# Kernel tuning notes

Hardware: AMD Instinct MI355X
Metric: run time of the kernel (lower is better)

Reference implementation:

```python
import jax, jax.numpy as jnp
import numpy as np

D = 192      # d_model
DE = 96      # d_edge
H = 8        # n_heads
DH = D // H  # d_head = 24
DF = 2 * D   # ff hidden = 384
N = 25000
E = 400000


def _layernorm(x, s, b, eps=1e-5):
    m = jnp.mean(x, axis=-1, keepdims=True)
    v = jnp.var(x, axis=-1, keepdims=True)
    return (x - m) * jax.lax.rsqrt(v + eps) * s + b


def setup_inputs() -> dict:
    key = jax.random.key(0)
    ks = jax.random.split(key, 12)
    sc = lambda d: 1.0 / np.sqrt(d)
    inp = {
        "x": jax.random.normal(ks[0], (N, D), jnp.float32),
        "edge_feat": jax.random.normal(ks[1], (E, DE), jnp.float32),
        "edge_index": jax.random.randint(ks[2], (2, E), 0, N, jnp.int64),
        # attention projections (stored [d_in, d_out], applied as x @ W)
        "Wq": jax.random.normal(ks[3], (D, D), jnp.float32) * sc(D),
        "Wk": jax.random.normal(ks[4], (D, D), jnp.float32) * sc(D),
        "Wv": jax.random.normal(ks[5], (D, D), jnp.float32) * sc(D),
        "We": jax.random.normal(ks[6], (DE, H), jnp.float32) * sc(DE),
        "Wo": jax.random.normal(ks[7], (D, D), jnp.float32) * sc(D),
        "bo": jnp.zeros((D,), jnp.float32),
        "Wg": jax.random.normal(ks[8], (2 * D, D), jnp.float32) * sc(2 * D),
        "bg": jnp.zeros((D,), jnp.float32),
        "ln1_s": jnp.ones((D,), jnp.float32),
        "ln1_b": jnp.zeros((D,), jnp.float32),
        "Wf1": jax.random.normal(ks[9], (D, DF), jnp.float32) * sc(D),
        "bf1": jnp.zeros((DF,), jnp.float32),
        "Wf2": jax.random.normal(ks[10], (DF, D), jnp.float32) * sc(DF),
        "bf2": jnp.zeros((D,), jnp.float32),
        "ln2_s": jnp.ones((D,), jnp.float32),
        "ln2_b": jnp.zeros((D,), jnp.float32),
    }
    return inp


def reference(x, edge_feat, edge_index, Wq, Wk, Wv, We, Wo, bo, Wg, bg,
              ln1_s, ln1_b, Wf1, bf1, Wf2, bf2, ln2_s, ln2_b):
    src, dst = edge_index[0], edge_index[1]
    n = x.shape[0]
    # per-edge gathered projections: [E, H, DH]
    q = (x[dst] @ Wq).reshape(-1, H, DH)
    k = (x[src] @ Wk).reshape(-1, H, DH)
    v = (x[src] @ Wv).reshape(-1, H, DH)
    score = jnp.sum(q * k, axis=-1) / np.sqrt(DH) + edge_feat @ We  # [E, H]
    # segment softmax over incoming edges of each dst node
    mx = jax.ops.segment_max(score, dst, num_segments=n)           # [N, H]
    alpha = jnp.exp(score - mx[dst])                                # [E, H]
    den = jax.ops.segment_sum(alpha, dst, num_segments=n)          # [N, H]
    num = jax.ops.segment_sum(alpha[..., None] * v, dst, num_segments=n)  # [N, H, DH]
    agg = (num / (den[:, :, None] + 1e-8)).reshape(n, D)
    o = agg @ Wo + bo
    g = jax.nn.sigmoid(jnp.concatenate([o, x], axis=-1) @ Wg + bg)
    y = _layernorm(g * o + (1.0 - g) * x, ln1_s, ln1_b)
    ff = jax.nn.silu(y @ Wf1 + bf1) @ Wf2 + bf2
    return _layernorm(y + ff, ln2_s, ln2_b)
```

## Files before the change

kernel.cpp:

```cpp
#include <hip/hip_runtime.h>
#include <cstdint>
#include <cstddef>

#define LOG2E 1.4426950408889634f

constexpr int Dm  = 192;
constexpr int DEe = 96;

typedef unsigned short u16;
typedef __attribute__((ext_vector_type(8))) short short8v;
typedef __attribute__((ext_vector_type(4))) float f32x4;

__device__ __forceinline__ u16 f2bf(float f) {
    uint32_t u = __builtin_bit_cast(uint32_t, f);
    uint32_t r = (u + 0x7FFF + ((u >> 16) & 1)) >> 16;
    return (u16)r;
}
__device__ __forceinline__ float bf2f(u16 h) {
    uint32_t u = ((uint32_t)h) << 16;
    return __builtin_bit_cast(float, u);
}
__device__ __forceinline__ uint32_t cvtpk_bf16(float lo, float hi) {
    uint32_t r;
    asm("v_cvt_pk_bf16_f32 %0, %1, %2" : "=v"(r) : "v"(lo), "v"(hi));
    return r;
}

__global__ void zero_ints(int* __restrict__ p, int n) {
    int i = blockIdx.x * blockDim.x + threadIdx.x;
    if (i < n) p[i] = 0;
}

__global__ __launch_bounds__(1024) void scan_kernel(const int* __restrict__ deg, int N,
                                                    int* __restrict__ offs) {
    __shared__ int sp[1024];
    int t = threadIdx.x;
    int per = (N + 1023) >> 10;
    int base = t * per;
    int sum = 0;
    for (int i = 0; i < per; ++i) {
        int idx = base + i;
        if (idx < N) sum += deg[idx];
    }
    sp[t] = sum;
    __syncthreads();
    for (int off = 1; off < 1024; off <<= 1) {
        int v = (t >= off) ? sp[t - off] : 0;
        __syncthreads();
        sp[t] += v;
        __syncthreads();
    }
    int run = sp[t] - sum;
    for (int i = 0; i < per; ++i) {
        int idx = base + i;
        if (idx < N) { offs[idx] = run; run += deg[idx]; }
    }
    if (t == 1023) offs[N] = sp[1023];
}

__global__ __launch_bounds__(256) void prepA(
    const int* __restrict__ ei, int E,
    const float* __restrict__ x, int n4, u16* __restrict__ xb,
    const float* __restrict__ Wq, const float* __restrict__ Wk,
    const float* __restrict__ Wv, const float* __restrict__ Wo,
    const float* __restrict__ Wg, const float* __restrict__ Wf1,
    const float* __restrict__ Wf2,
    u16* __restrict__ Wqkvt, u16* __restrict__ Wot,
    u16* __restrict__ Wgt, u16* __restrict__ Wf1t, u16* __restrict__ Wf2t,
    int* __restrict__ deg)
{
    int i = blockIdx.x * 256 + threadIdx.x;
    if (i < E) {
        atomicAdd(&deg[ei[E + i]], 1);
        return;
    }
    i -= E;
    if (i < n4) {
        float4 v = ((const float4*)x)[i];
        uint32_t p0 = cvtpk_bf16(v.x, v.y);
        uint32_t p1 = cvtpk_bf16(v.z, v.w);
        ushort4 o;
        o.x = (u16)(p0 & 0xffff); o.y = (u16)(p0 >> 16);
        o.z = (u16)(p1 & 0xffff); o.w = (u16)(p1 >> 16);
        ((ushort4*)xb)[i] = o;
        return;
    }
    int idx = i - n4;
    if (idx < 110592) {
        int n = idx / 192, k = idx % 192;
        const float* W = n < 192 ? Wq : (n < 384 ? Wk : Wv);
        Wqkvt[idx] = f2bf(W[(size_t)k * 192 + (n % 192)]);
    } else if (idx < 147456) {
        int j = idx - 110592;
        int n = j / 192, k = j % 192;
        Wot[j] = f2bf(Wo[(size_t)k * 192 + n]);
    } else if (idx < 221184) {
        int j = idx - 147456;
        int n = j / 384, k = j % 384;
        Wgt[j] = f2bf(Wg[(size_t)k * 192 + n]);
    } else if (idx < 294912) {
        int j = idx - 221184;
        int n = j / 192, k = j % 192;
        Wf1t[j] = f2bf(Wf1[(size_t)k * 384 + n]);
    } else if (idx < 368640) {
        int j = idx - 294912;
        int n = j / 384, k = j % 384;
        Wf2t[j] = f2bf(Wf2[(size_t)k * 192 + n]);
    }
}

__global__ __launch_bounds__(256) void phaseC(
    int EB,
    const int* __restrict__ ei, int E,
    const float* __restrict__ ef, const float* __restrict__ We,
    const int* __restrict__ offs, int* __restrict__ cur,
    float* __restrict__ scb, int* __restrict__ sbuf,
    const u16* __restrict__ xb, int M, int gm64,
    const u16* __restrict__ Wt, u16* __restrict__ qkvb)
{
    int bid = blockIdx.x;
    int tid = threadIdx.x;
    if (bid < EB) {
        __shared__ float We_s[DEe * 8];
        __shared__ float ef_s[32][100];
        for (int i = tid; i < DEe * 8; i += 256) We_s[i] = We[i];
        int e0 = bid * 32;
        #pragma unroll
        for (int rep = 0; rep < 3; ++rep) {
            int idx = tid + 256 * rep;
            int el = idx / 24, c4 = idx % 24;
            int e = e0 + el;
            float4 v = make_float4(0.f, 0.f, 0.f, 0.f);
            if (e < E) v = *(const float4*)&ef[(size_t)e * DEe + c4 * 4];
            *(float4*)&ef_s[el][c4 * 4] = v;
        }
        __syncthreads();
        int el = tid >> 3, h = tid & 7;
        int e = e0 + el;
        if (e >= E) return;
        float epj = 0.f;
        #pragma unroll 8
        for (int i = 0; i < DEe; ++i) epj += ef_s[el][i] * We_s[i * 8 + h];

        int lane = tid & 63;
        int pos = 0;
        if (h == 0) {
            int dst = ei[E + e];
            pos = offs[dst] + atomicAdd(&cur[dst], 1);
        }
        pos = __shfl(pos, lane & 56, 64);
        scb[(size_t)pos * 8 + h] = epj * LOG2E;
        if (h == 0) sbuf[pos] = ei[e];
        return;
    }

    int qb = bid - EB;
    int m0 = (qb % gm64) * 64, n0 = (qb / gm64) * 192;
    int w = tid >> 6, lane = tid & 63;
    int c16 = lane & 15, hi2 = lane >> 4, kof = hi2 * 8;

    int rcm[4];
    #pragma unroll
    for (int mr = 0; mr < 4; ++mr) {
        int r = m0 + mr * 16 + c16;
        rcm[mr] = r < M ? r : M - 1;
    }

    f32x4 acc[4][3];
    #pragma unroll
    for (int mr = 0; mr < 4; ++mr)
        #pragma unroll
        for (int nr = 0; nr < 3; ++nr) acc[mr][nr] = (f32x4)(0.f);

    #pragma unroll 1
    for (int ks = 0; ks < 6; ++ks) {
        short8v af[4], bfr[3];
        #pragma unroll
        for (int mr = 0; mr < 4; ++mr)
            af[mr] = *(const short8v*)(xb + (size_t)rcm[mr] * 192 + ks * 32 + kof);
        #pragma unroll
        for (int nr = 0; nr < 3; ++nr)
            bfr[nr] = *(const short8v*)(Wt + (size_t)(n0 + w * 48 + nr * 16 + c16) * 192 + ks * 32 + kof);
        #pragma unroll
        for (int mr = 0; mr < 4; ++mr)
            #pragma unroll
            for (int nr = 0; nr < 3; ++nr)
                acc[mr][nr] = __builtin_amdgcn_mfma_f32_16x16x32_bf16(
                    af[mr], bfr[nr], acc[mr][nr], 0, 0, 0);
    }

    #pragma unroll
    for (int mr = 0; mr < 4; ++mr)
        #pragma unroll
        for (int nr = 0; nr < 3; ++nr) {
            uint32_t p0 = cvtpk_bf16(acc[mr][nr][0], acc[mr][nr][1]);
            uint32_t p1 = cvtpk_bf16(acc[mr][nr][2], acc[mr][nr][3]);
            int r0 = m0 + mr * 16 + hi2 * 4;
            int col = n0 + w * 48 + nr * 16 + c16;
            if (r0     < M) qkvb[(size_t)(r0    ) * 576 + col] = (u16)(p0 & 0xffff);
            if (r0 + 1 < M) qkvb[(size_t)(r0 + 1) * 576 + col] = (u16)(p0 >> 16);
            if (r0 + 2 < M) qkvb[(size_t)(r0 + 2) * 576 + col] = (u16)(p1 & 0xffff);
            if (r0 + 3 < M) qkvb[(size_t)(r0 + 3) * 576 + col] = (u16)(p1 >> 16);
        }
}

__global__ __launch_bounds__(256) void agg_fused(
    const u16* __restrict__ qkv, const float* __restrict__ scb,
    const int* __restrict__ sbuf, const int* __restrict__ offs,
    int N, u16* __restrict__ aggb)
{
    int node = blockIdx.x * 4 + (threadIdx.x >> 6);
    if (node >= N) return;
    int lane = threadIdx.x & 63;
    int h = lane >> 3;
    int di = (3 * lane) >> 1;
    int odd = lane & 1;

    int beg = offs[node], end = offs[node + 1];
    u16* og = aggb + (size_t)node * Dm;
    int b0 = 3 * lane;
    if (beg >= end) {
        og[b0] = 0; og[b0 + 1] = 0; og[b0 + 2] = 0;
        return;
    }

    const uint32_t* qrow = (const uint32_t*)(qkv + (size_t)node * 576);
    uint32_t qd0 = qrow[di], qd1 = qrow[di + 1];
    float q0, q1, q2;
    if (!odd) { q0 = bf2f(qd0 & 0xffff); q1 = bf2f(qd0 >> 16); q2 = bf2f(qd1 & 0xffff); }
    else      { q0 = bf2f(qd0 >> 16);    q1 = bf2f(qd1 & 0xffff); q2 = bf2f(qd1 >> 16); }

    auto clampi = [&](int i) { return i < end ? i : end - 1; };

    float den = 0.f, a0 = 0.f, a1 = 0.f, a2 = 0.f;

    uint32_t ck[2][2], cv[2][2]; float cep[2];
    uint32_t nk[2][2], nv[2][2]; float nep[2];
    int s0, s1;

    {
        int p00 = clampi(beg),     p01 = clampi(beg + 1);
        int p10 = clampi(beg + 2), p11 = clampi(beg + 3);
        int sA = sbuf[p00], sB = sbuf[p01], sC = sbuf[p10], sD = sbuf[p11];
        const uint32_t* r;
        r = (const uint32_t*)(qkv + (size_t)sA * 576 + 192);
        ck[0][0] = r[di]; ck[0][1] = r[di + 1];
        r = (const uint32_t*)(qkv + (size_t)sA * 576 + 384);
        cv[0][0] = r[di]; cv[0][1] = r[di + 1];
        r = (const uint32_t*)(qkv + (size_t)sB * 576 + 192);
        ck[1][0] = r[di]; ck[1][1] = r[di + 1];
        r = (const uint32_t*)(qkv + (size_t)sB * 576 + 384);
        cv[1][0] = r[di]; cv[1][1] = r[di + 1];
        r = (const uint32_t*)(qkv + (size_t)sC * 576 + 192);
        nk[0][0] = r[di]; nk[0][1] = r[di + 1];
        r = (const uint32_t*)(qkv + (size_t)sC * 576 + 384);
        nv[0][0] = r[di]; nv[0][1] = r[di + 1];
        r = (const uint32_t*)(qkv + (size_t)sD * 576 + 192);
        nk[1][0] = r[di]; nk[1][1] = r[di + 1];
        r = (const uint32_t*)(qkv + (size_t)sD * 576 + 384);
        nv[1][0] = r[di]; nv[1][1] = r[di + 1];
        cep[0] = scb[(size_t)p00 * 8 + h]; cep[1] = scb[(size_t)p01 * 8 + h];
        nep[0] = scb[(size_t)p10 * 8 + h]; nep[1] = scb[(size_t)p11 * 8 + h];
        s0 = sbuf[clampi(beg + 4)]; s1 = sbuf[clampi(beg + 5)];
    }

    for (int idx = beg; idx < end; idx += 2) {
        #pragma unroll
        for (int j = 0; j < 2; ++j) {
            float k0, k1, k2, v0, v1, v2;
            uint32_t kd0 = ck[j][0], kd1 = ck[j][1];
            uint32_t vd0 = cv[j][0], vd1 = cv[j][1];
            if (!odd) {
                k0 = bf2f(kd0 & 0xffff); k1 = bf2f(kd0 >> 16); k2 = bf2f(kd1 & 0xffff);
                v0 = bf2f(vd0 & 0xffff); v1 = bf2f(vd0 >> 16); v2 = bf2f(vd1 & 0xffff);
            } else {
                k0 = bf2f(kd0 >> 16); k1 = bf2f(kd1 & 0xffff); k2 = bf2f(kd1 >> 16);
                v0 = bf2f(vd0 >> 16); v1 = bf2f(vd1 & 0xffff); v2 = bf2f(vd1 >> 16);
            }
            float pd = q0 * k0 + q1 * k1 + q2 * k2;
            pd += __shfl_xor(pd, 1, 64);
            pd += __shfl_xor(pd, 2, 64);
            pd += __shfl_xor(pd, 4, 64);
            float p = exp2f(pd * 0.2944885836f + cep[j]);
            if (idx + j < end) {
                den += p;
                a0 += p * v0; a1 += p * v1; a2 += p * v2;
            }
        }
        #pragma unroll
        for (int j = 0; j < 2; ++j) {
            ck[j][0] = nk[j][0]; ck[j][1] = nk[j][1];
            cv[j][0] = nv[j][0]; cv[j][1] = nv[j][1];
            cep[j] = nep[j];
        }
        {
            const uint32_t* r;
            r = (const uint32_t*)(qkv + (size_t)s0 * 576 + 192);
            nk[0][0] = r[di]; nk[0][1] = r[di + 1];
            r = (const uint32_t*)(qkv + (size_t)s0 * 576 + 384);
            nv[0][0] = r[di]; nv[0][1] = r[di + 1];
            r = (const uint32_t*)(qkv + (size_t)s1 * 576 + 192);
            nk[1][0] = r[di]; nk[1][1] = r[di + 1];
            r = (const uint32_t*)(qkv + (size_t)s1 * 576 + 384);
            nv[1][0] = r[di]; nv[1][1] = r[di + 1];
            nep[0] = scb[(size_t)clampi(idx + 4) * 8 + h];
            nep[1] = scb[(size_t)clampi(idx + 5) * 8 + h];
        }
        s0 = sbuf[clampi(idx + 6)]; s1 = sbuf[clampi(idx + 7)];
    }

    float rden = 1.f / (den + 1e-8f);
    og[b0]     = f2bf(a0 * rden);
    og[b0 + 1] = f2bf(a1 * rden);
    og[b0 + 2] = f2bf(a2 * rden);
}

__global__ __launch_bounds__(512) void chain_fused(
    const u16* __restrict__ aggb, const u16* __restrict__ xb, int M,
    const u16* __restrict__ Wot, const float* __restrict__ bo,
    const u16* __restrict__ Wgt, const float* __restrict__ bg,
    const float* __restrict__ l1s, const float* __restrict__ l1b,
    const u16* __restrict__ Wf1t, const float* __restrict__ bf1,
    const u16* __restrict__ Wf2t, const float* __restrict__ bf2,
    const float* __restrict__ l2s, const float* __restrict__ l2b,
    float* __restrict__ out)
{
    __shared__ __align__(16) short Ybuf[128 * 200];
    __shared__ __align__(16) short Fbuf[128 * 392];
    __shared__ float red[2][4][128];

    int tid = threadIdx.x;
    int m0 = blockIdx.x * 128;
    int w = tid >> 6, lane = tid & 63;
    int wr = w >> 2, wc = w & 3;
    int c16 = lane & 15, hi2 = lane >> 4, kof = hi2 * 8;
    int rbase = m0 + wr * 64;
    int lbase = wr * 64;

    int rcm[4];
    #pragma unroll
    for (int mr = 0; mr < 4; ++mr) {
        int r = rbase + mr * 16 + c16;
        rcm[mr] = r < M ? r : M - 1;
    }

    f32x4 oacc[4][3];
    #pragma unroll
    for (int mr = 0; mr < 4; ++mr)
        #pragma unroll
        for (int nr = 0; nr < 3; ++nr) oacc[mr][nr] = (f32x4)(0.f);
    #pragma unroll 1
    for (int ks = 0; ks < 6; ++ks) {
        short8v af[4], bfr[3];
        #pragma unroll
        for (int mr = 0; mr < 4; ++mr)
            af[mr] = *(const short8v*)(aggb + (size_t)rcm[mr] * 192 + ks * 32 + kof);
        #pragma unroll
        for (int nr = 0; nr < 3; ++nr)
            bfr[nr] = *(const short8v*)(Wot + (size_t)(wc * 48 + nr * 16 + c16) * 192 + ks * 32 + kof);
        #pragma unroll
        for (int mr = 0; mr < 4; ++mr)
            #pragma unroll
            for (int nr = 0; nr < 3; ++nr)
                oacc[mr][nr] = __builtin_amdgcn_mfma_f32_16x16x32_bf16(
                    af[mr], bfr[nr], oacc[mr][nr], 0, 0, 0);
    }
    #pragma unroll
    for (int nr = 0; nr < 3; ++nr) {
        int col = wc * 48 + nr * 16 + c16;
        float b = bo[col];
        #pragma unroll
        for (int mr = 0; mr < 4; ++mr) {
            #pragma unroll
            for (int reg = 0; reg < 4; ++reg) oacc[mr][nr][reg] += b;
            uint32_t p0 = cvtpk_bf16(oacc[mr][nr][0], oacc[mr][nr][1]);
            uint32_t p1 = cvtpk_bf16(oacc[mr][nr][2], oacc[mr][nr][3]);
            int row0 = lbase + mr * 16 + hi2 * 4;
            Ybuf[(row0    ) * 200 + col] = (short)(p0 & 0xffff);
            Ybuf[(row0 + 1) * 200 + col] = (short)(p0 >> 16);
            Ybuf[(row0 + 2) * 200 + col] = (short)(p1 & 0xffff);
            Ybuf[(row0 + 3) * 200 + col] = (short)(p1 >> 16);
        }
    }
    __syncthreads();

    f32x4 zacc[4][3];
    #pragma unroll
    for (int mr = 0; mr < 4; ++mr)
        #pragma unroll
        for (int nr = 0; nr < 3; ++nr) zacc[mr][nr] = (f32x4)(0.f);
    #pragma unroll 1
    for (int ks = 0; ks < 6; ++ks) {
        short8v af[4], bfr[3];
        #pragma unroll
        for (int mr = 0; mr < 4; ++mr)
            af[mr] = *(const short8v*)&Ybuf[(lbase + mr * 16 + c16) * 200 + ks * 32 + kof];
        #pragma unroll
        for (int nr = 0; nr < 3; ++nr)
            bfr[nr] = *(const short8v*)(Wgt + (size_t)(wc * 48 + nr * 16 + c16) * 384 + ks * 32 + kof);
        #pragma unroll
        for (int mr = 0; mr < 4; ++mr)
            #pragma unroll
            for (int nr = 0; nr < 3; ++nr)
                zacc[mr][nr] = __builtin_amdgcn_mfma_f32_16x16x32_bf16(
                    af[mr], bfr[nr], zacc[mr][nr], 0, 0, 0);
    }
    #pragma unroll 1
    for (int ks = 0; ks < 6; ++ks) {
        short8v af[4], bfr[3];
        #pragma unroll
        for (int mr = 0; mr < 4; ++mr)
            af[mr] = *(const short8v*)(xb + (size_t)rcm[mr] * 192 + ks * 32 + kof);
        #pragma unroll
        for (int nr = 0; nr < 3; ++nr)
            bfr[nr] = *(const short8v*)(Wgt + (size_t)(wc * 48 + nr * 16 + c16) * 384 + 192 + ks * 32 + kof);
        #pragma unroll
        for (int mr = 0; mr < 4; ++mr)
            #pragma unroll
            for (int nr = 0; nr < 3; ++nr)
                zacc[mr][nr] = __builtin_amdgcn_mfma_f32_16x16x32_bf16(
                    af[mr], bfr[nr], zacc[mr][nr], 0, 0, 0);
    }
    float s1p[4][4], s2p[4][4];
    #pragma unroll
    for (int mr = 0; mr < 4; ++mr)
        #pragma unroll
        for (int reg = 0; reg < 4; ++reg) {
            int gr = rbase + mr * 16 + hi2 * 4 + reg;
            int rcR = gr < M ? gr : M - 1;
            float s1 = 0.f, s2 = 0.f;
            #pragma unroll
            for (int nr = 0; nr < 3; ++nr) {
                int col = wc * 48 + nr * 16 + c16;
                float z = zacc[mr][nr][reg] + bg[col];
                float g = 1.f / (1.f + expf(-z));
                float xv = bf2f(xb[(size_t)rcR * 192 + col]);
                float val = g * oacc[mr][nr][reg] + (1.f - g) * xv;
                zacc[mr][nr][reg] = val;
                s1 += val; s2 += val * val;
            }
            #pragma unroll
            for (int mS = 1; mS < 16; mS <<= 1) {
                s1 += __shfl_xor(s1, mS, 64);
                s2 += __shfl_xor(s2, mS, 64);
            }
            s1p[mr][reg] = s1; s2p[mr][reg] = s2;
        }
    if (c16 == 0) {
        #pragma unroll
        for (int mr = 0; mr < 4; ++mr)
            #pragma unroll
            for (int reg = 0; reg < 4; ++reg) {
                int rowIdx = lbase + mr * 16 + hi2 * 4 + reg;
                red[0][wc][rowIdx] = s1p[mr][reg];
                red[1][wc][rowIdx] = s2p[mr][reg];
            }
    }
    __syncthreads();
    #pragma unroll
    for (int mr = 0; mr < 4; ++mr)
        #pragma unroll
        for (int reg = 0; reg < 4; ++reg) {
            int rowIdx = lbase + mr * 16 + hi2 * 4 + reg;
            float S1 = red[0][0][rowIdx] + red[0][1][rowIdx] + red[0][2][rowIdx] + red[0][3][rowIdx];
            float S2 = red[1][0][rowIdx] + red[1][1][rowIdx] + red[1][2][rowIdx] + red[1][3][rowIdx];
            float mean = S1 * (1.f / 192.f);
            float var  = S2 * (1.f / 192.f) - mean * mean;
            float inv  = rsqrtf(var + 1e-5f);
            #pragma unroll
            for (int nr = 0; nr < 3; ++nr) {
                int col = wc * 48 + nr * 16 + c16;
                float yv = (zacc[mr][nr][reg] - mean) * inv * l1s[col] + l1b[col];
                Ybuf[rowIdx * 200 + col] = (short)f2bf(yv);
            }
        }
    __syncthreads();

    f32x4 tacc[4][6];
    #pragma unroll
    for (int mr = 0; mr < 4; ++mr)
        #pragma unroll
        for (int nr = 0; nr < 6; ++nr) tacc[mr][nr] = (f32x4)(0.f);
    #pragma unroll 1
    for (int ks = 0; ks < 6; ++ks) {
        short8v af[4], bfr[6];
        #pragma unroll
        for (int mr = 0; mr < 4; ++mr)
            af[mr] = *(const short8v*)&Ybuf[(lbase + mr * 16 + c16) * 200 + ks * 32 + kof];
        #pragma unroll
        for (int nr = 0; nr < 6; ++nr)
            bfr[nr] = *(const short8v*)(Wf1t + (size_t)(wc * 96 + nr * 16 + c16) * 192 + ks * 32 + kof);
        #pragma unroll
        for (int mr = 0; mr < 4; ++mr)
            #pragma unroll
            for (int nr = 0; nr < 6; ++nr)
                tacc[mr][nr] = __builtin_amdgcn_mfma_f32_16x16x32_bf16(
                    af[mr], bfr[nr], tacc[mr][nr], 0, 0, 0);
    }
    #pragma unroll
    for (int nr = 0; nr < 6; ++nr) {
        int col = wc * 96 + nr * 16 + c16;
        float b = bf1[col];
        #pragma unroll
        for (int mr = 0; mr < 4; ++mr) {
            float t0[4];
            #pragma unroll
            for (int reg = 0; reg < 4; ++reg) {
                float z = tacc[mr][nr][reg] + b;
                t0[reg] = z / (1.f + expf(-z));
            }
            uint32_t p0 = cvtpk_bf16(t0[0], t0[1]);
            uint32_t p1 = cvtpk_bf16(t0[2], t0[3]);
            int row0 = lbase + mr * 16 + hi2 * 4;
            Fbuf[(row0    ) * 392 + col] = (short)(p0 & 0xffff);
            Fbuf[(row0 + 1) * 392 + col] = (short)(p0 >> 16);
            Fbuf[(row0 + 2) * 392 + col] = (short)(p1 & 0xffff);
            Fbuf[(row0 + 3) * 392 + col] = (short)(p1 >> 16);
        }
    }
    __syncthreads();

    f32x4 facc[4][3];
    #pragma unroll
    for (int mr = 0; mr < 4; ++mr)
        #pragma unroll
        for (int nr = 0; nr < 3; ++nr) facc[mr][nr] = (f32x4)(0.f);
    #pragma unroll 1
    for (int ks = 0; ks < 12; ++ks) {
        short8v af[4], bfr[3];
        #pragma unroll
        for (int mr = 0; mr < 4; ++mr)
            af[mr] = *(const short8v*)&Fbuf[(lbase + mr * 16 + c16) * 392 + ks * 32 + kof];
        #pragma unroll
        for (int nr = 0; nr < 3; ++nr)
            bfr[nr] = *(const short8v*)(Wf2t + (size_t)(wc * 48 + nr * 16 + c16) * 384 + ks * 32 + kof);
        #pragma unroll
        for (int mr = 0; mr < 4; ++mr)
            #pragma unroll
            for (int nr = 0; nr < 3; ++nr)
                facc[mr][nr] = __builtin_amdgcn_mfma_f32_16x16x32_bf16(
                    af[mr], bfr[nr], facc[mr][nr], 0, 0, 0);
    }
    float s1q[4][4], s2q[4][4];
    #pragma unroll
    for (int mr = 0; mr < 4; ++mr)
        #pragma unroll
        for (int reg = 0; reg < 4; ++reg) {
            int rowIdx = lbase + mr * 16 + hi2 * 4 + reg;
            float s1 = 0.f, s2 = 0.f;
            #pragma unroll
            for (int nr = 0; nr < 3; ++nr) {
                int col = wc * 48 + nr * 16 + c16;
                float val = facc[mr][nr][reg] + bf2[col] + bf2f((u16)Ybuf[rowIdx * 200 + col]);
                facc[mr][nr][reg] = val;
                s1 += val; s2 += val * val;
            }
            #pragma unroll
            for (int mS = 1; mS < 16; mS <<= 1) {
                s1 += __shfl_xor(s1, mS, 64);
                s2 += __shfl_xor(s2, mS, 64);
            }
            s1q[mr][reg] = s1; s2q[mr][reg] = s2;
        }
    if (c16 == 0) {
        #pragma unroll
        for (int mr = 0; mr < 4; ++mr)
            #pragma unroll
            for (int reg = 0; reg < 4; ++reg) {
                int rowIdx = lbase + mr * 16 + hi2 * 4 + reg;
                red[0][wc][rowIdx] = s1q[mr][reg];
                red[1][wc][rowIdx] = s2q[mr][reg];
            }
    }
    __syncthreads();
    #pragma unroll
    for (int mr = 0; mr < 4; ++mr)
        #pragma unroll
        for (int reg = 0; reg < 4; ++reg) {
            int rowIdx = lbase + mr * 16 + hi2 * 4 + reg;
            int r = m0 + rowIdx;
            if (r >= M) continue;
            float S1 = red[0][0][rowIdx] + red[0][1][rowIdx] + red[0][2][rowIdx] + red[0][3][rowIdx];
            float S2 = red[1][0][rowIdx] + red[1][1][rowIdx] + red[1][2][rowIdx] + red[1][3][rowIdx];
            float mean = S1 * (1.f / 192.f);
            float var  = S2 * (1.f / 192.f) - mean * mean;
            float inv  = rsqrtf(var + 1e-5f);
            #pragma unroll
            for (int nr = 0; nr < 3; ++nr) {
                int col = wc * 48 + nr * 16 + c16;
                out[(size_t)r * 192 + col] =
                    (facc[mr][nr][reg] - mean) * inv * l2s[col] + l2b[col];
            }
        }
}

extern "C" void kernel_launch(void* const* d_in, const int* in_sizes, int n_in,
                              void* d_out, int out_size, void* d_ws, size_t ws_size,
                              hipStream_t stream) {
    const float* x   = (const float*)d_in[0];
    const float* ef  = (const float*)d_in[1];
    const int*   ei  = (const int*)d_in[2];
    const float* Wq  = (const float*)d_in[3];
    const float* Wk  = (const float*)d_in[4];
    const float* Wv  = (const float*)d_in[5];
    const float* We  = (const float*)d_in[6];
    const float* Wo  = (const float*)d_in[7];
    const float* bo  = (const float*)d_in[8];
    const float* Wg  = (const float*)d_in[9];
    const float* bg  = (const float*)d_in[10];
    const float* l1s = (const float*)d_in[11];
    const float* l1b = (const float*)d_in[12];
    const float* Wf1 = (const float*)d_in[13];
    const float* bf1 = (const float*)d_in[14];
    const float* Wf2 = (const float*)d_in[15];
    const float* bf2 = (const float*)d_in[16];
    const float* l2s = (const float*)d_in[17];
    const float* l2b = (const float*)d_in[18];

    int N = in_sizes[0] / Dm;
    int E = in_sizes[1] / DEe;
    float* out = (float*)d_out;

    char* wp = (char*)d_ws;
    auto alloc = [&](size_t bytes) -> void* {
        void* p = wp;
        wp += (bytes + 255) & ~(size_t)255;
        return p;
    };
    size_t NF = (size_t)N * Dm;
    u16*   xb     = (u16*)alloc(NF * 2);
    u16*   qkvb   = (u16*)alloc((size_t)N * 576 * 2);
    u16*   aggb   = (u16*)alloc(NF * 2);
    float* scb    = (float*)alloc((size_t)E * 8 * 4);
    int*   sbuf   = (int*)  alloc((size_t)E * 4);
    int*   degcur = (int*)  alloc((size_t)2 * N * 4);
    int*   offs   = (int*)  alloc((size_t)(N + 1) * 4);
    u16*   Wqkvt  = (u16*)alloc((size_t)576 * 192 * 2);
    u16*   Wot    = (u16*)alloc((size_t)192 * 192 * 2);
    u16*   Wgt    = (u16*)alloc((size_t)192 * 384 * 2);
    u16*   Wf1t   = (u16*)alloc((size_t)384 * 192 * 2);
    u16*   Wf2t   = (u16*)alloc((size_t)192 * 384 * 2);
    int* deg = degcur;
    int* cur = degcur + N;

    int gm64  = (N + 63) / 64;
    int gm128 = (N + 127) / 128;
    int n4 = N * Dm / 4;

    zero_ints<<<dim3((2 * N + 255) / 256), 256, 0, stream>>>(degcur, 2 * N);

    int prepTotal = E + n4 + 368640;
    prepA<<<dim3((prepTotal + 255) / 256), 256, 0, stream>>>(
        ei, E, x, n4, xb, Wq, Wk, Wv, Wo, Wg, Wf1, Wf2,
        Wqkvt, Wot, Wgt, Wf1t, Wf2t, deg);

    scan_kernel<<<dim3(1), 1024, 0, stream>>>(deg, N, offs);

    int EB = (E + 31) / 32;
    int QB = gm64 * 3;
    phaseC<<<dim3(EB + QB), 256, 0, stream>>>(EB,
        ei, E, ef, We, offs, cur, scb, sbuf,
        xb, N, gm64, Wqkvt, qkvb);

    agg_fused<<<dim3((N + 3) / 4), 256, 0, stream>>>(qkvb, scb, sbuf, offs, N, aggb);

    chain_fused<<<dim3(gm128), 512, 0, stream>>>(aggb, xb, N,
        Wot, bo, Wgt, bg, l1s, l1b, Wf1t, bf1, Wf2t, bf2, l2s, l2b, out);
}
```

Before: 272.5 us.

## Split phaseC into separate QKV GEMM and register-based edge score kernels

The combined phaseC launch, which handled the edge-score blocks and the QKV GEMM blocks in one grid, is split into two launches: a 2D-grid qkv_gemm and an edge_fused kernel. The edge kernel no longer stages edge features in shared memory. Each of 8 lanes per edge loads 12 features straight into registers, computes partial sums for all 8 heads against a permuted, LOG2E-prescaled We in shared memory, then combines them with a butterfly shuffle reduction. This removes a syncthreads and the shared staging of edge features, at the cost of an extra kernel launch and no longer overlapping the GEMM with the edge work.

```diff
diff --git a/kernel.cpp b/kernel.cpp
--- a/kernel.cpp
+++ b/kernel.cpp
@@ -109,53 +109,87 @@
     }
 }
 
-__global__ __launch_bounds__(256) void phaseC(
-    int EB,
+__global__ __launch_bounds__(256) void edge_fused(
     const int* __restrict__ ei, int E,
     const float* __restrict__ ef, const float* __restrict__ We,
     const int* __restrict__ offs, int* __restrict__ cur,
-    float* __restrict__ scb, int* __restrict__ sbuf,
-    const u16* __restrict__ xb, int M, int gm64,
+    float* __restrict__ scb, int* __restrict__ sbuf)
+{
+    __shared__ float We_s[96 * 12];
+    int tid = threadIdx.x;
+    for (int i = tid; i < 768; i += 256) {
+        int kk = i >> 3, h = i & 7;
+        int r = (kk % 12) * 8 + kk / 12;
+        We_s[r * 12 + h] = We[kk * 8 + h] * LOG2E;
+    }
+    __syncthreads();
+
+    int lane = tid & 63, w = tid >> 6;
+    int sub = lane & 7, eg = lane >> 3;
+    int e = blockIdx.x * 32 + w * 8 + eg;
+    if (e >= E) return;
+
+    int pos = 0;
+    if (sub == 0) {
+        int src = ei[e];
+        int dst = ei[E + e];
+        pos = offs[dst] + atomicAdd(&cur[dst], 1);
+        sbuf[pos] = src;
+    }
+
+    const float* er = ef + (size_t)e * 96 + sub * 12;
+    float4 f0 = *(const float4*)(er);
+    float4 f1 = *(const float4*)(er + 4);
+    float4 f2 = *(const float4*)(er + 8);
+    float fv[12] = {f0.x, f0.y, f0.z, f0.w,
+                    f1.x, f1.y, f1.z, f1.w,
+                    f2.x, f2.y, f2.z, f2.w};
+
+    float acc[8];
+    #pragma unroll
+    for (int h = 0; h < 8; ++h) acc[h] = 0.f;
+    #pragma unroll
+    for (int k = 0; k < 12; ++k) {
+        const float* wr = &We_s[(k * 8 + sub) * 12];
+        float4 wa = *(const float4*)(wr);
+        float4 wb = *(const float4*)(wr + 4);
+        acc[0] = fmaf(fv[k], wa.x, acc[0]);
+        acc[1] = fmaf(fv[k], wa.y, acc[1]);
+        acc[2] = fmaf(fv[k], wa.z, acc[2]);
+        acc[3] = fmaf(fv[k], wa.w, acc[3]);
+        acc[4] = fmaf(fv[k], wb.x, acc[4]);
+        acc[5] = fmaf(fv[k], wb.y, acc[5]);
+        acc[6] = fmaf(fv[k], wb.z, acc[6]);
+        acc[7] = fmaf(fv[k], wb.w, acc[7]);
+    }
+
+    float t8[8];
+    #pragma unroll
+    for (int h = 0; h < 8; ++h) t8[h] = acc[h] + __shfl_xor(acc[h], 1, 64);
+    float t4[4];
+    #pragma unroll
+    for (int j = 0; j < 4; ++j) {
+        float v = (sub & 1) ? t8[2 * j + 1] : t8[2 * j];
+        t4[j] = v + __shfl_xor(v, 2, 64);
+    }
+    float t2[2];
+    #pragma unroll
+    for (int i2 = 0; i2 < 2; ++i2) {
+        float v = (sub & 2) ? t4[2 * i2 + 1] : t4[2 * i2];
+        t2[i2] = v + __shfl_xor(v, 4, 64);
+    }
+    float sc = (sub & 4) ? t2[1] : t2[0];
+
+    int pb = __shfl(pos, lane & 56, 64);
+    scb[(size_t)pb * 8 + sub] = sc;
+}
+
+__global__ __launch_bounds__(256) void qkv_gemm(
+    const u16* __restrict__ xb, int M,
     const u16* __restrict__ Wt, u16* __restrict__ qkvb)
 {
-    int bid = blockIdx.x;
     int tid = threadIdx.x;
-    if (bid < EB) {
-        __shared__ float We_s[DEe * 8];
-        __shared__ float ef_s[32][100];
-        for (int i = tid; i < DEe * 8; i += 256) We_s[i] = We[i];
-        int e0 = bid * 32;
-        #pragma unroll
-        for (int rep = 0; rep < 3; ++rep) {
-            int idx = tid + 256 * rep;
-            int el = idx / 24, c4 = idx % 24;
-            int e = e0 + el;
-            float4 v = make_float4(0.f, 0.f, 0.f, 0.f);
-            if (e < E) v = *(const float4*)&ef[(size_t)e * DEe + c4 * 4];
-            *(float4*)&ef_s[el][c4 * 4] = v;
-        }
-        __syncthreads();
-        int el = tid >> 3, h = tid & 7;
-        int e = e0 + el;
-        if (e >= E) return;
-        float epj = 0.f;
-        #pragma unroll 8
-        for (int i = 0; i < DEe; ++i) epj += ef_s[el][i] * We_s[i * 8 + h];
-
-        int lane = tid & 63;
-        int pos = 0;
-        if (h == 0) {
-            int dst = ei[E + e];
-            pos = offs[dst] + atomicAdd(&cur[dst], 1);
-        }
-        pos = __shfl(pos, lane & 56, 64);
-        scb[(size_t)pos * 8 + h] = epj * LOG2E;
-        if (h == 0) sbuf[pos] = ei[e];
-        return;
-    }
-
-    int qb = bid - EB;
-    int m0 = (qb % gm64) * 64, n0 = (qb / gm64) * 192;
+    int m0 = blockIdx.x * 64, n0 = blockIdx.y * 192;
     int w = tid >> 6, lane = tid & 63;
     int c16 = lane & 15, hi2 = lane >> 4, kof = hi2 * 8;
 
@@ -656,11 +690,10 @@
 
     scan_kernel<<<dim3(1), 1024, 0, stream>>>(deg, N, offs);
 
-    int EB = (E + 31) / 32;
-    int QB = gm64 * 3;
-    phaseC<<<dim3(EB + QB), 256, 0, stream>>>(EB,
-        ei, E, ef, We, offs, cur, scb, sbuf,
-        xb, N, gm64, Wqkvt, qkvb);
+    qkv_gemm<<<dim3(gm64, 3), 256, 0, stream>>>(xb, N, Wqkvt, qkvb);
+
+    edge_fused<<<dim3((E + 31) / 32), 256, 0, stream>>>(ei, E, ef, We,
+        offs, cur, scb, sbuf);
 
     agg_fused<<<dim3((N + 3) / 4), 256, 0, stream>>>(qkvb, scb, sbuf, offs, N, aggb);
 
```

New measurement: 275.3 us (median of 2 runs). About the same (+1.1%).
